# Kernel optimization log

Hardware: AMD Instinct MI355X
Metric: run time of the kernel (lower is better)

## Reference

```python
import jax, jax.numpy as jnp
import numpy as np

NUM_HEADS = 8


def _attn(q, k, v, scale):
    # q: [B,H,Nq,d], k/v: [B,H,Nk,d]
    a = jax.nn.softmax(jnp.einsum('bhqd,bhkd->bhqk', q, k) * scale, axis=-1)
    return jnp.einsum('bhqk,bhkd->bhqd', a, v)


def setup_inputs() -> dict:
    key = jax.random.key(0)
    k1, k2, k3 = jax.random.split(key, 3)
    B, N, C = 8, 1024, 768
    x = jax.random.normal(k1, (B, N, C), dtype=jnp.float32)
    w_qkv = jax.random.normal(k2, (3 * C, C), dtype=jnp.float32) * 0.02
    w_proj = jax.random.normal(k3, (C, C), dtype=jnp.float32) * 0.02
    b_proj = jnp.zeros((C,), dtype=jnp.float32)
    return {"x": x, "w_qkv": w_qkv, "w_proj": w_proj, "b_proj": b_proj}


def reference(x, w_qkv, w_proj, b_proj):
    B, N, C = x.shape
    H = NUM_HEADS
    hd = C // H            # full head dim (scale uses this, per the source)
    g = hd // 3            # per-group head dim
    scale = hd ** (-0.5)

    qkv = (x @ w_qkv.T).reshape(B, N, 3, H, hd).transpose(2, 0, 3, 1, 4)  # [3,B,H,N,hd]
    q, k, v = qkv[0], qkv[1], qkv[2]

    q3, q4, q5 = q[..., :g], q[..., g:2 * g], q[..., 2 * g:]
    k3, k4, k5 = k[..., :g], k[..., g:2 * g], k[..., 2 * g:]
    v3, v4, v5 = v[..., :g], v[..., g:2 * g], v[..., 2 * g:]

    def merge(o):  # [B,H,N,g] -> [B,N,H*g]
        return o.transpose(0, 2, 1, 3).reshape(B, N, C // 3)

    x3 = merge(_attn(q4, jnp.concatenate([k3, k4], axis=2), jnp.concatenate([v3, v4], axis=2), scale))
    x4 = merge(_attn(q5, jnp.concatenate([k3, k5], axis=2), jnp.concatenate([v3, v5], axis=2), scale))
    x5 = merge(_attn(q5, jnp.concatenate([k4, k5], axis=2), jnp.concatenate([v4, v5], axis=2), scale))

    out = jnp.concatenate([x3, x4, x5], axis=2)
    return out @ w_proj.T + b_proj
```

## Files before the change

kernel.cpp:

```cpp
#include <hip/hip_runtime.h>
#include <hip/hip_bf16.h>

typedef unsigned short u16;
typedef __attribute__((ext_vector_type(8))) short short8;
typedef __attribute__((ext_vector_type(4))) float f32x4;

__device__ __forceinline__ u16 f2b(float f) {
  union { float f; unsigned u; } a; a.f = f;
  unsigned r = a.u + 0x7fffu + ((a.u >> 16) & 1u);
  return (u16)(r >> 16);
}

__device__ __forceinline__ unsigned pkbf16(float lo, float hi) {
  unsigned r;
  asm("v_cvt_pk_bf16_f32 %0, %1, %2" : "=v"(r) : "v"(lo), "v"(hi));
  return r;
}

#define GLD_LDS16(gp, lp) __builtin_amdgcn_global_load_lds( \
    (const __attribute__((address_space(1))) void*)(gp),    \
    (__attribute__((address_space(3))) void*)(lp), 16, 0, 0)

__global__ __launch_bounds__(256) void cvt3(
    const float* __restrict__ x, const float* __restrict__ wq, const float* __restrict__ wp,
    u16* __restrict__ xb, u16* __restrict__ wqb, u16* __restrict__ wpb)
{
  const int NX = 8192 * 768 / 4, NQ = 2304 * 768 / 4, NP = 768 * 768 / 4;
  int i = blockIdx.x * 256 + threadIdx.x;
  if (i < NX) {
    float4 v = *(const float4*)&x[(size_t)i * 4];
    u16 o[4] = { f2b(v.x), f2b(v.y), f2b(v.z), f2b(v.w) };
    *(uint2*)&xb[(size_t)i * 4] = *(uint2*)o;
  } else if (i < NX + NQ) {
    int j = i - NX;
    float sc = (j < 147456) ? 0.14724447f : 1.0f;
    float4 v = *(const float4*)&wq[(size_t)j * 4];
    u16 o[4] = { f2b(v.x * sc), f2b(v.y * sc), f2b(v.z * sc), f2b(v.w * sc) };
    *(uint2*)&wqb[(size_t)j * 4] = *(uint2*)o;
  } else if (i < NX + NQ + NP) {
    int j = i - NX - NQ;
    int oo = (j * 4) / 768, ii = (j * 4) % 768;
    int a = ii >> 8, h = (ii >> 5) & 7, c = ii & 31;
    float4 v = *(const float4*)&wp[(size_t)j * 4];
    u16 o[4] = { f2b(v.x), f2b(v.y), f2b(v.z), f2b(v.w) };
    *(uint2*)&wpb[oo * 768 + h * 96 + a * 32 + c] = *(uint2*)o;
  }
}

__global__ __launch_bounds__(256) void gemm_bt(
    const u16* __restrict__ A, const u16* __restrict__ Bt,
    u16* __restrict__ Cb, float* __restrict__ Cf, const float* __restrict__ bias,
    int M, int N, int K)
{
  __shared__ u16 Al[128 * 32];
  __shared__ u16 Bl[128 * 32];
  const int tid = threadIdx.x;
  const int lane = tid & 63, wave = tid >> 6;
  const int wr = wave >> 1, wc = wave & 1;
  const int g = lane >> 4, c16 = lane & 15;
  const int m0 = blockIdx.y * 128, n0 = blockIdx.x * 128;

  f32x4 acc[4][4] = {};

  const int c0 = tid, c1 = tid + 256;
  const int r0 = c0 >> 2, o0 = (c0 & 3) * 8;
  const int r1 = c1 >> 2, o1 = (c1 & 3) * 8;
  const u16* a0 = A + (size_t)(m0 + r0) * K + o0;
  const u16* a1 = A + (size_t)(m0 + r1) * K + o1;
  const u16* b0 = Bt + (size_t)(n0 + r0) * K + o0;
  const u16* b1 = Bt + (size_t)(n0 + r1) * K + o1;

  for (int k0 = 0; k0 < K; k0 += 32) {
    GLD_LDS16(a0 + k0, Al + c0 * 8);
    GLD_LDS16(a1 + k0, Al + c1 * 8);
    GLD_LDS16(b0 + k0, Bl + c0 * 8);
    GLD_LDS16(b1 + k0, Bl + c1 * 8);
    __syncthreads();
    short8 af[4], bfr[4];
#pragma unroll
    for (int m = 0; m < 4; ++m)
      af[m] = *(const short8*)&Al[(wr * 64 + m * 16 + c16) * 32 + g * 8];
#pragma unroll
    for (int n = 0; n < 4; ++n)
      bfr[n] = *(const short8*)&Bl[(wc * 64 + n * 16 + c16) * 32 + g * 8];
#pragma unroll
    for (int m = 0; m < 4; ++m)
#pragma unroll
      for (int n = 0; n < 4; ++n)
        acc[m][n] = __builtin_amdgcn_mfma_f32_16x16x32_bf16(af[m], bfr[n], acc[m][n], 0, 0, 0);
    __syncthreads();
  }

  if (Cb) {
#pragma unroll
    for (int m = 0; m < 4; ++m) {
      const int row = m0 + wr * 64 + m * 16 + g * 4;
#pragma unroll
      for (int n = 0; n < 4; ++n) {
        const int col = n0 + wc * 64 + n * 16 + c16;
#pragma unroll
        for (int j = 0; j < 4; ++j)
          Cb[(size_t)(row + j) * N + col] = f2b(acc[m][n][j]);
      }
    }
  } else {
#pragma unroll
    for (int m = 0; m < 4; ++m) {
      const int row = m0 + wr * 64 + m * 16 + g * 4;
#pragma unroll
      for (int n = 0; n < 4; ++n) {
        const int col = n0 + wc * 64 + n * 16 + c16;
        const float bb = bias[col];
#pragma unroll
        for (int j = 0; j < 4; ++j)
          Cf[(size_t)(row + j) * N + col] = acc[m][n][j] + bb;
      }
    }
  }
}

__global__ __launch_bounds__(256) void vtrans(const u16* __restrict__ qkv, u16* __restrict__ vt)
{
  __shared__ u16 Vtl[96 * 72];
  const int tid = threadIdx.x;
  const int bh = blockIdx.x >> 4, nt = blockIdx.x & 15;
  const int b = bh >> 3, h = bh & 7;
  const int n0 = nt * 64;
  const size_t tb = (size_t)b * 1024;
#pragma unroll
  for (int i = 0; i < 3; ++i) {
    int c = tid + i * 256;
    int key = c / 12, cc = c % 12;
    uint4 v = *(const uint4*)&qkv[(tb + n0 + key) * 2304 + 1536 + h * 96 + cc * 8];
    union { uint4 u; u16 s[8]; } cv; cv.u = v;
#pragma unroll
    for (int j = 0; j < 8; ++j)
      Vtl[(cc * 8 + j) * 72 + key] = cv.s[j];
  }
  __syncthreads();
#pragma unroll
  for (int i = 0; i < 3; ++i) {
    int c = tid + i * 256;
    int d = c >> 3, c2 = c & 7;
    int chunk = c2 >> 2;
    int kA = ((c2 & 1) << 4) | ((c2 & 2) << 1);
    const u16* src = &Vtl[d * 72 + c2 * 8];
    size_t base = ((size_t)bh * 96 + d) * 1024 + n0 + chunk * 32;
    *(uint2*)&vt[base + kA]     = *(const uint2*)(src);
    *(uint2*)&vt[base + kA + 8] = *(const uint2*)(src + 4);
  }
}

__global__ __launch_bounds__(256, 2) void attn_kernel(
    const u16* __restrict__ qkv, const u16* __restrict__ vt, u16* __restrict__ feat)
{
  __shared__ u16 smem[3 * 64 * 40 + 96 * 72];
  u16* Kl = smem;
  u16* Vl = smem + 3 * 64 * 40;

  const int tid = threadIdx.x;
  const int lane = tid & 63, wave = tid >> 6;
  const int g = lane >> 4, c16 = lane & 15;
  const int id = blockIdx.x;
  const int h = id & 7, qt = (id >> 3) & 15, b = id >> 7;
  const int bh = b * 8 + h;
  const int q0 = qt * 64 + wave * 16;
  const size_t tb = (size_t)b * 1024;

  short8 qf[2];
#pragma unroll
  for (int qs = 0; qs < 2; ++qs)
    qf[qs] = *(const short8*)&qkv[(tb + q0 + c16) * 2304 + h * 96 + 32 + 32 * qs + 8 * g];

  short8 ones;
#pragma unroll
  for (int i = 0; i < 8; ++i) ones[i] = (short)0x3F80;

  f32x4 acc[4][2] = {};
  f32x4 lsv[4] = {};

  int kk_key[3], kk_cc[3], vv_d[3], vv_c[3];
#pragma unroll
  for (int i = 0; i < 3; ++i) {
    int c = tid + i * 256;
    kk_key[i] = c / 12; kk_cc[i] = c % 12;
    vv_d[i] = c >> 3;   vv_c[i] = c & 7;
  }
  uint4 kst[3], vst[3];
#pragma unroll
  for (int i = 0; i < 3; ++i) {
    kst[i] = *(const uint4*)&qkv[(tb + kk_key[i]) * 2304 + 768 + h * 96 + kk_cc[i] * 8];
    vst[i] = *(const uint4*)&vt[((size_t)bh * 96 + vv_d[i]) * 1024 + vv_c[i] * 8];
  }

  const int ATT[5] = {0, 0, 1, 3, 2};
  const int QS[5]  = {0, 0, 1, 1, 1};
  const int KS[5]  = {0, 1, 0, 2, 1};

  for (int t = 0; t < 16; ++t) {
    __syncthreads();
#pragma unroll
    for (int i = 0; i < 3; ++i) {
      int part = kk_cc[i] >> 2, g4 = kk_cc[i] & 3;
      *(uint4*)&Kl[part * 2560 + kk_key[i] * 40 + g4 * 8] = kst[i];
      *(uint4*)&Vl[vv_d[i] * 72 + vv_c[i] * 8] = vst[i];
    }
    if (t < 15) {
      int kv0 = (t + 1) * 64;
#pragma unroll
      for (int i = 0; i < 3; ++i) {
        kst[i] = *(const uint4*)&qkv[(tb + kv0 + kk_key[i]) * 2304 + 768 + h * 96 + kk_cc[i] * 8];
        vst[i] = *(const uint4*)&vt[((size_t)bh * 96 + vv_d[i]) * 1024 + kv0 + vv_c[i] * 8];
      }
    }
    __syncthreads();

#pragma unroll
    for (int u = 0; u < 5; ++u) {
      const int att = ATT[u], qs = QS[u], ks = KS[u];
      short8 kf[4];
#pragma unroll
      for (int n = 0; n < 4; ++n)
        kf[n] = *(const short8*)&Kl[ks * 2560 + (n * 16 + c16) * 40 + g * 8];

      const f32x4 z = {0.f, 0.f, 0.f, 0.f};
      f32x4 St[4];
      __builtin_amdgcn_s_setprio(1);
#pragma unroll
      for (int n = 0; n < 4; ++n)
        St[n] = __builtin_amdgcn_mfma_f32_16x16x32_bf16(kf[n], qf[qs], z, 0, 0, 0);
      __builtin_amdgcn_s_setprio(0);
      short8 vf[2][2];
#pragma unroll
      for (int n = 0; n < 2; ++n)
#pragma unroll
        for (int kk = 0; kk < 2; ++kk)
          vf[n][kk] = *(const short8*)&Vl[(ks * 32 + n * 16 + c16) * 72 + kk * 32 + g * 8];
      short8 pa[2];
#pragma unroll
      for (int kk = 0; kk < 2; ++kk) {
        union { unsigned u[4]; short8 s; } w;
        w.u[0] = pkbf16(__builtin_amdgcn_exp2f(St[2 * kk][0]),     __builtin_amdgcn_exp2f(St[2 * kk][1]));
        w.u[1] = pkbf16(__builtin_amdgcn_exp2f(St[2 * kk][2]),     __builtin_amdgcn_exp2f(St[2 * kk][3]));
        w.u[2] = pkbf16(__builtin_amdgcn_exp2f(St[2 * kk + 1][0]), __builtin_amdgcn_exp2f(St[2 * kk + 1][1]));
        w.u[3] = pkbf16(__builtin_amdgcn_exp2f(St[2 * kk + 1][2]), __builtin_amdgcn_exp2f(St[2 * kk + 1][3]));
        pa[kk] = w.s;
      }
      __builtin_amdgcn_s_setprio(1);
#pragma unroll
      for (int n = 0; n < 2; ++n)
#pragma unroll
        for (int kk = 0; kk < 2; ++kk)
          acc[att][n] = __builtin_amdgcn_mfma_f32_16x16x32_bf16(pa[kk], vf[n][kk], acc[att][n], 0, 0, 0);
#pragma unroll
      for (int kk = 0; kk < 2; ++kk)
        lsv[att] = __builtin_amdgcn_mfma_f32_16x16x32_bf16(pa[kk], ones, lsv[att], 0, 0, 0);
      __builtin_amdgcn_s_setprio(0);
    }
  }

  lsv[1] += lsv[3];
  lsv[2] += lsv[3];
#pragma unroll
  for (int n = 0; n < 2; ++n) {
    acc[1][n] += acc[3][n];
    acc[2][n] += acc[3][n];
  }

  __syncthreads();
  u16* Ol = smem + wave * 1536;
#pragma unroll
  for (int a = 0; a < 3; ++a) {
    f32x4 inv;
#pragma unroll
    for (int r = 0; r < 4; ++r) inv[r] = 1.0f / lsv[a][r];
#pragma unroll
    for (int n = 0; n < 2; ++n)
#pragma unroll
      for (int r = 0; r < 4; ++r)
        Ol[(g * 4 + r) * 96 + a * 32 + n * 16 + c16] = f2b(acc[a][n][r] * inv[r]);
  }
#pragma unroll
  for (int i = 0; i < 3; ++i) {
    int chunk = lane + 64 * i;
    int row = chunk / 12, cc = chunk % 12;
    uint4 val = *(const uint4*)&Ol[row * 96 + cc * 8];
    *(uint4*)&feat[(tb + q0 + row) * 768 + h * 96 + cc * 8] = val;
  }
}

extern "C" void kernel_launch(void* const* d_in, const int* in_sizes, int n_in,
                              void* d_out, int out_size, void* d_ws, size_t ws_size,
                              hipStream_t stream) {
  const float* x  = (const float*)d_in[0];
  const float* wq = (const float*)d_in[1];
  const float* wp = (const float*)d_in[2];
  const float* bp = (const float*)d_in[3];
  float* out = (float*)d_out;

  char* ws = (char*)d_ws;
  u16* xb    = (u16*)(ws);
  u16* wqb   = (u16*)(ws + 12582912);
  u16* wpb   = (u16*)(ws + 16121856);
  u16* qkvb  = (u16*)(ws + 17301504);
  u16* vtb   = (u16*)(ws + 55050240);
  u16* featb = xb;

  cvt3<<<8448, 256, 0, stream>>>(x, wq, wp, xb, wqb, wpb);
  gemm_bt<<<dim3(18, 64), 256, 0, stream>>>(xb, wqb, qkvb, nullptr, nullptr, 8192, 2304, 768);
  vtrans<<<1024, 256, 0, stream>>>(qkvb, vtb);
  attn_kernel<<<1024, 256, 0, stream>>>(qkvb, vtb, featb);
  gemm_bt<<<dim3(6, 64), 256, 0, stream>>>(featb, wpb, nullptr, out, bp, 8192, 768, 768);
}
```

Before: 206.6 us.

## Process 32 query rows per wave in attention to reuse K/V tiles

Each wave in the attention kernel now handles two 16-row query sub-tiles instead of one, so a block covers 128 queries and the grid is halved. K and V fragments loaded from LDS, and the staged K/V global loads, are shared across twice as many queries, which cuts LDS and global traffic per query. In exchange, accumulator registers double, which may lower occupancy, and fewer blocks run. The bf16 packing in the conversion kernels is also rewritten as cosmetic cleanup.

```diff
diff --git a/kernel.cpp b/kernel.cpp
--- a/kernel.cpp
+++ b/kernel.cpp
@@ -4,10 +4,11 @@
 typedef unsigned short u16;
 typedef __attribute__((ext_vector_type(8))) short short8;
 typedef __attribute__((ext_vector_type(4))) float f32x4;
+typedef __attribute__((ext_vector_type(4))) unsigned uint32x4;
 
 __device__ __forceinline__ u16 f2b(float f) {
-  union { float f; unsigned u; } a; a.f = f;
-  unsigned r = a.u + 0x7fffu + ((a.u >> 16) & 1u);
+  unsigned u = __builtin_bit_cast(unsigned, f);
+  unsigned r = u + 0x7fffu + ((u >> 16) & 1u);
   return (u16)(r >> 16);
 }
 
@@ -29,21 +30,26 @@
   int i = blockIdx.x * 256 + threadIdx.x;
   if (i < NX) {
     float4 v = *(const float4*)&x[(size_t)i * 4];
-    u16 o[4] = { f2b(v.x), f2b(v.y), f2b(v.z), f2b(v.w) };
-    *(uint2*)&xb[(size_t)i * 4] = *(uint2*)o;
+    u16 o0 = f2b(v.x), o1 = f2b(v.y), o2 = f2b(v.z), o3 = f2b(v.w);
+    unsigned lo = (unsigned)o0 | ((unsigned)o1 << 16);
+    unsigned hi = (unsigned)o2 | ((unsigned)o3 << 16);
+    uint2 pk; pk.x = lo; pk.y = hi;
+    *(uint2*)&xb[(size_t)i * 4] = pk;
   } else if (i < NX + NQ) {
     int j = i - NX;
     float sc = (j < 147456) ? 0.14724447f : 1.0f;
     float4 v = *(const float4*)&wq[(size_t)j * 4];
-    u16 o[4] = { f2b(v.x * sc), f2b(v.y * sc), f2b(v.z * sc), f2b(v.w * sc) };
-    *(uint2*)&wqb[(size_t)j * 4] = *(uint2*)o;
+    u16 o0 = f2b(v.x * sc), o1 = f2b(v.y * sc), o2 = f2b(v.z * sc), o3 = f2b(v.w * sc);
+    uint2 pk; pk.x = (unsigned)o0 | ((unsigned)o1 << 16); pk.y = (unsigned)o2 | ((unsigned)o3 << 16);
+    *(uint2*)&wqb[(size_t)j * 4] = pk;
   } else if (i < NX + NQ + NP) {
     int j = i - NX - NQ;
     int oo = (j * 4) / 768, ii = (j * 4) % 768;
     int a = ii >> 8, h = (ii >> 5) & 7, c = ii & 31;
     float4 v = *(const float4*)&wp[(size_t)j * 4];
-    u16 o[4] = { f2b(v.x), f2b(v.y), f2b(v.z), f2b(v.w) };
-    *(uint2*)&wpb[oo * 768 + h * 96 + a * 32 + c] = *(uint2*)o;
+    u16 o0 = f2b(v.x), o1 = f2b(v.y), o2 = f2b(v.z), o3 = f2b(v.w);
+    uint2 pk; pk.x = (unsigned)o0 | ((unsigned)o1 << 16); pk.y = (unsigned)o2 | ((unsigned)o3 << 16);
+    *(uint2*)&wpb[oo * 768 + h * 96 + a * 32 + c] = pk;
   }
 }
 
@@ -131,11 +137,10 @@
   for (int i = 0; i < 3; ++i) {
     int c = tid + i * 256;
     int key = c / 12, cc = c % 12;
-    uint4 v = *(const uint4*)&qkv[(tb + n0 + key) * 2304 + 1536 + h * 96 + cc * 8];
-    union { uint4 u; u16 s[8]; } cv; cv.u = v;
+    short8 v = *(const short8*)&qkv[(tb + n0 + key) * 2304 + 1536 + h * 96 + cc * 8];
 #pragma unroll
     for (int j = 0; j < 8; ++j)
-      Vtl[(cc * 8 + j) * 72 + key] = cv.s[j];
+      Vtl[(cc * 8 + j) * 72 + key] = (u16)v[j];
   }
   __syncthreads();
 #pragma unroll
@@ -162,22 +167,24 @@
   const int lane = tid & 63, wave = tid >> 6;
   const int g = lane >> 4, c16 = lane & 15;
   const int id = blockIdx.x;
-  const int h = id & 7, qt = (id >> 3) & 15, b = id >> 7;
+  const int h = id & 7, qt = (id >> 3) & 7, b = id >> 6;
   const int bh = b * 8 + h;
-  const int q0 = qt * 64 + wave * 16;
+  const int q0 = qt * 128 + wave * 32;
   const size_t tb = (size_t)b * 1024;
 
-  short8 qf[2];
+  short8 qf[2][2];
 #pragma unroll
   for (int qs = 0; qs < 2; ++qs)
-    qf[qs] = *(const short8*)&qkv[(tb + q0 + c16) * 2304 + h * 96 + 32 + 32 * qs + 8 * g];
+#pragma unroll
+    for (int m = 0; m < 2; ++m)
+      qf[qs][m] = *(const short8*)&qkv[(tb + q0 + m * 16 + c16) * 2304 + h * 96 + 32 + 32 * qs + 8 * g];
 
   short8 ones;
 #pragma unroll
   for (int i = 0; i < 8; ++i) ones[i] = (short)0x3F80;
 
-  f32x4 acc[4][2] = {};
-  f32x4 lsv[4] = {};
+  f32x4 acc[4][2][2] = {};
+  f32x4 lsv[4][2] = {};
 
   int kk_key[3], kk_cc[3], vv_d[3], vv_c[3];
 #pragma unroll
@@ -218,70 +225,78 @@
 #pragma unroll
     for (int u = 0; u < 5; ++u) {
       const int att = ATT[u], qs = QS[u], ks = KS[u];
-      short8 kf[4];
+      short8 kf[4], vf[2][2];
 #pragma unroll
       for (int n = 0; n < 4; ++n)
         kf[n] = *(const short8*)&Kl[ks * 2560 + (n * 16 + c16) * 40 + g * 8];
-
-      const f32x4 z = {0.f, 0.f, 0.f, 0.f};
-      f32x4 St[4];
-      __builtin_amdgcn_s_setprio(1);
-#pragma unroll
-      for (int n = 0; n < 4; ++n)
-        St[n] = __builtin_amdgcn_mfma_f32_16x16x32_bf16(kf[n], qf[qs], z, 0, 0, 0);
-      __builtin_amdgcn_s_setprio(0);
-      short8 vf[2][2];
 #pragma unroll
       for (int n = 0; n < 2; ++n)
 #pragma unroll
         for (int kk = 0; kk < 2; ++kk)
           vf[n][kk] = *(const short8*)&Vl[(ks * 32 + n * 16 + c16) * 72 + kk * 32 + g * 8];
-      short8 pa[2];
-#pragma unroll
-      for (int kk = 0; kk < 2; ++kk) {
-        union { unsigned u[4]; short8 s; } w;
-        w.u[0] = pkbf16(__builtin_amdgcn_exp2f(St[2 * kk][0]),     __builtin_amdgcn_exp2f(St[2 * kk][1]));
-        w.u[1] = pkbf16(__builtin_amdgcn_exp2f(St[2 * kk][2]),     __builtin_amdgcn_exp2f(St[2 * kk][3]));
-        w.u[2] = pkbf16(__builtin_amdgcn_exp2f(St[2 * kk + 1][0]), __builtin_amdgcn_exp2f(St[2 * kk + 1][1]));
-        w.u[3] = pkbf16(__builtin_amdgcn_exp2f(St[2 * kk + 1][2]), __builtin_amdgcn_exp2f(St[2 * kk + 1][3]));
-        pa[kk] = w.s;
+
+      const f32x4 z = {0.f, 0.f, 0.f, 0.f};
+#pragma unroll
+      for (int m = 0; m < 2; ++m) {
+        f32x4 St[4];
+        __builtin_amdgcn_s_setprio(1);
+#pragma unroll
+        for (int n = 0; n < 4; ++n)
+          St[n] = __builtin_amdgcn_mfma_f32_16x16x32_bf16(kf[n], qf[qs][m], z, 0, 0, 0);
+        __builtin_amdgcn_s_setprio(0);
+        short8 pa[2];
+#pragma unroll
+        for (int kk = 0; kk < 2; ++kk) {
+          uint32x4 w;
+          w.x = pkbf16(__builtin_amdgcn_exp2f(St[2 * kk][0]),     __builtin_amdgcn_exp2f(St[2 * kk][1]));
+          w.y = pkbf16(__builtin_amdgcn_exp2f(St[2 * kk][2]),     __builtin_amdgcn_exp2f(St[2 * kk][3]));
+          w.z = pkbf16(__builtin_amdgcn_exp2f(St[2 * kk + 1][0]), __builtin_amdgcn_exp2f(St[2 * kk + 1][1]));
+          w.w = pkbf16(__builtin_amdgcn_exp2f(St[2 * kk + 1][2]), __builtin_amdgcn_exp2f(St[2 * kk + 1][3]));
+          pa[kk] = __builtin_bit_cast(short8, w);
+        }
+        __builtin_amdgcn_s_setprio(1);
+#pragma unroll
+        for (int n = 0; n < 2; ++n)
+#pragma unroll
+          for (int kk = 0; kk < 2; ++kk)
+            acc[att][m][n] = __builtin_amdgcn_mfma_f32_16x16x32_bf16(pa[kk], vf[n][kk], acc[att][m][n], 0, 0, 0);
+#pragma unroll
+        for (int kk = 0; kk < 2; ++kk)
+          lsv[att][m] = __builtin_amdgcn_mfma_f32_16x16x32_bf16(pa[kk], ones, lsv[att][m], 0, 0, 0);
+        __builtin_amdgcn_s_setprio(0);
       }
-      __builtin_amdgcn_s_setprio(1);
+    }
+  }
+
+#pragma unroll
+  for (int m = 0; m < 2; ++m) {
+    lsv[1][m] += lsv[3][m];
+    lsv[2][m] += lsv[3][m];
+#pragma unroll
+    for (int n = 0; n < 2; ++n) {
+      acc[1][m][n] += acc[3][m][n];
+      acc[2][m][n] += acc[3][m][n];
+    }
+  }
+
+  __syncthreads();
+  u16* Ol = smem + wave * 3072;
+#pragma unroll
+  for (int a = 0; a < 3; ++a)
+#pragma unroll
+    for (int m = 0; m < 2; ++m) {
+      f32x4 inv;
+#pragma unroll
+      for (int r = 0; r < 4; ++r) inv[r] = 1.0f / lsv[a][m][r];
 #pragma unroll
       for (int n = 0; n < 2; ++n)
 #pragma unroll
-        for (int kk = 0; kk < 2; ++kk)
-          acc[att][n] = __builtin_amdgcn_mfma_f32_16x16x32_bf16(pa[kk], vf[n][kk], acc[att][n], 0, 0, 0);
-#pragma unroll
-      for (int kk = 0; kk < 2; ++kk)
-        lsv[att] = __builtin_amdgcn_mfma_f32_16x16x32_bf16(pa[kk], ones, lsv[att], 0, 0, 0);
-      __builtin_amdgcn_s_setprio(0);
-    }
-  }
-
-  lsv[1] += lsv[3];
-  lsv[2] += lsv[3];
-#pragma unroll
-  for (int n = 0; n < 2; ++n) {
-    acc[1][n] += acc[3][n];
-    acc[2][n] += acc[3][n];
-  }
-
-  __syncthreads();
-  u16* Ol = smem + wave * 1536;
-#pragma unroll
-  for (int a = 0; a < 3; ++a) {
-    f32x4 inv;
-#pragma unroll
-    for (int r = 0; r < 4; ++r) inv[r] = 1.0f / lsv[a][r];
-#pragma unroll
-    for (int n = 0; n < 2; ++n)
-#pragma unroll
-      for (int r = 0; r < 4; ++r)
-        Ol[(g * 4 + r) * 96 + a * 32 + n * 16 + c16] = f2b(acc[a][n][r] * inv[r]);
-  }
-#pragma unroll
-  for (int i = 0; i < 3; ++i) {
+        for (int r = 0; r < 4; ++r)
+          Ol[(m * 16 + g * 4 + r) * 96 + a * 32 + n * 16 + c16] = f2b(acc[a][m][n][r] * inv[r]);
+    }
+  __builtin_amdgcn_s_barrier();
+#pragma unroll
+  for (int i = 0; i < 6; ++i) {
     int chunk = lane + 64 * i;
     int row = chunk / 12, cc = chunk % 12;
     uint4 val = *(const uint4*)&Ol[row * 96 + cc * 8];
@@ -309,6 +324,6 @@
   cvt3<<<8448, 256, 0, stream>>>(x, wq, wp, xb, wqb, wpb);
   gemm_bt<<<dim3(18, 64), 256, 0, stream>>>(xb, wqb, qkvb, nullptr, nullptr, 8192, 2304, 768);
   vtrans<<<1024, 256, 0, stream>>>(qkvb, vtb);
-  attn_kernel<<<1024, 256, 0, stream>>>(qkvb, vtb, featb);
+  attn_kernel<<<512, 256, 0, stream>>>(qkvb, vtb, featb);
   gemm_bt<<<dim3(6, 64), 256, 0, stream>>>(featb, wpb, nullptr, out, bp, 8192, 768, 768);
 }
```

After: 167.1 us. 19.2% less time.
